# Performance work log

Measured on AMD Instinct MI355X. Metric: run time of the kernel, lower is better.

## Reference

```python
import jax, jax.numpy as jnp
import numpy as np

NT, NS, NH, NG, NR, NC = 365, 300, 128, 32, 8, 1


def _linear_params(key, fin, fout):
    k1, k2 = jax.random.split(key)
    s = 1.0 / np.sqrt(fin)
    W = jax.random.uniform(k1, (fout, fin), minval=-s, maxval=s, dtype=jnp.float32)
    b = jax.random.uniform(k2, (fout,), minval=-s, maxval=s, dtype=jnp.float32)
    return W, b


def setup_inputs() -> dict:
    key = jax.random.key(0)
    ks = jax.random.split(key, 9)
    x = jax.random.normal(ks[0], (NT, NS, 6), dtype=jnp.float32)
    xc = jax.random.normal(ks[1], (NS, NG), dtype=jnp.float32)
    fcR_w1, fcR_b1 = _linear_params(ks[2], NG, 256)
    fcR_w2, fcR_b2 = _linear_params(ks[3], 256, NH * NR)
    fcW_w1, fcW_b1 = _linear_params(ks[4], NG, 256)
    fcW_w2, fcW_b2 = _linear_params(ks[5], 256, NH * 7)
    fcT_w1, fcT_b1 = _linear_params(ks[6], 6 + NG, 256)
    fcT_w2, fcT_b2 = _linear_params(ks[7], 256, NH * 3)
    fcCT_w, fcCT_b = _linear_params(ks[8], 2 + NG, NC * NH * 3)
    return dict(x=x, xc=xc,
                fcR_w1=fcR_w1, fcR_b1=fcR_b1, fcR_w2=fcR_w2, fcR_b2=fcR_b2,
                fcW_w1=fcW_w1, fcW_b1=fcW_b1, fcW_w2=fcW_w2, fcW_b2=fcW_b2,
                fcT_w1=fcT_w1, fcT_b1=fcT_b1, fcT_w2=fcT_w2, fcT_b2=fcT_b2,
                fcCT_w=fcCT_w, fcCT_b=fcCT_b)


def _mlp(x, w1, b1, w2, b2):
    # Linear -> Tanh -> Dropout(identity in eval) -> Linear
    h = jnp.tanh(x @ w1.T + b1)
    return h @ w2.T + b2


def _conv_ts(q, r):
    # q: [nt, ns, nh]; r: [ns, nh, nr] routing weights. Causal temporal conv:
    # out[t] = sum_i q[t-i] * r[..., i]  (zero padded on the left)
    nt = q.shape[0]
    nr = r.shape[-1]
    qp = jnp.concatenate([jnp.zeros((nr - 1,) + q.shape[1:], q.dtype), q], axis=0)
    out = qp[nr - 1: nr - 1 + nt] * r[None, :, :, 0]
    for i in range(1, nr):
        out = out + qp[nr - 1 - i: nr - 1 - i + nt] * r[None, :, :, i]
    return out


def reference(x, xc, fcR_w1, fcR_b1, fcR_w2, fcR_b2,
              fcW_w1, fcW_b1, fcW_w2, fcW_b2,
              fcT_w1, fcT_b1, fcT_w2, fcT_b2,
              fcCT_w, fcCT_b):
    nh, nr = NH, NR
    P, E, T1, T2 = x[..., 0], x[..., 1], x[..., 2], x[..., 3]
    nt, ns = P.shape
    xcT = jnp.broadcast_to(xc[None], (nt, ns, xc.shape[-1]))
    xT = jnp.concatenate([x, xcT], axis=-1)                      # [nt, ns, 6+ng]

    # static gates per (site, bucket): sepPar with ['sigmoid']*4,'exp','relu','skip'
    w = _mlp(xc, fcW_w1, fcW_b1, fcW_w2, fcW_b2)                 # [ns, nh*7]
    kp = jax.nn.sigmoid(w[:, 0 * nh:1 * nh])
    ks_ = jax.nn.sigmoid(w[:, 1 * nh:2 * nh])
    kg = jax.nn.sigmoid(w[:, 2 * nh:3 * nh])
    gp = jax.nn.sigmoid(w[:, 3 * nh:4 * nh])
    gL = jnp.exp(w[:, 4 * nh:5 * nh]) * 2.0
    qb = jax.nn.relu(w[:, 5 * nh:6 * nh])
    ga = jax.nn.softmax(w[:, 6 * nh:7 * nh], axis=1)             # [ns, nh]

    # time-varying gates: ['skip','relu','exp']; vi overridden by hardsigmoid(v*2)
    v = _mlp(xT, fcT_w1, fcT_b1, fcT_w2, fcT_b2)                 # [nt, ns, nh*3]
    vi = jnp.clip(v[:, :, :nh] * 2.0 / 6.0 + 0.5, 0.0, 1.0)     # F.hardsigmoid(v*2)
    ve = jax.nn.relu(v[:, :, nh:2 * nh]) * 2.0
    vm = jnp.exp(v[:, :, 2 * nh:3 * nh])

    wR = _mlp(xc, fcR_w1, fcR_b1, fcR_w2, fcR_b2)                # [ns, nh*nr]
    r = jax.nn.relu(wR[:, :nh * nr]).reshape(ns, nh, nr)

    # snow fraction vf = arccos((T1+T2)/(T2-T1))/3.1415, overridden at extremes
    denom = T2 - T1
    ratio = jnp.clip((T1 + T2) / jnp.where(denom == 0, 1.0, denom), -1.0, 1.0)
    vf = jnp.arccos(ratio) / 3.1415
    vf = jnp.where(T1 >= 0, 0.0, jnp.where(T2 <= 0, 1.0, vf))
    Ps = P * vf                                                  # snow  [nt, ns]
    Pl = (P * (1.0 - vf))[:, :, None] * vi                       # rain  [nt, ns, nh]
    Ev = E[:, :, None] * ve                                      # evap  [nt, ns, nh]

    def step(carry, inp):
        Sf, Ss, Sg = carry
        Ps_k, Pl_k, Ev_k, vm_k = inp
        qf = jnp.minimum(Sf + Ps_k, vm_k)
        Sf = jax.nn.relu(Sf + Ps_k - vm_k)
        H = jax.nn.relu(Ss + Pl_k + qf - Ev_k)
        qp_ = jax.nn.relu(kp * (H - gL))
        qs = ks_ * jnp.minimum(H, gL)
        Ss = H - qp_ - qs
        qso = qs * (1.0 - gp)
        qsg = qs * gp
        qg = kg * (Sg + qsg) + qb
        Sg = (1.0 - kg) * (Sg + qsg) - qb
        return (Sf, Ss, Sg), (qp_, qso, qg)

    z = jnp.zeros((ns, nh), dtype=x.dtype)
    _, (Q1T, Q2T, Q3T) = jax.lax.scan(step, (z, z, z),
                                      (Ps[:, :, None], Pl, Ev, vm))

    Q1R = _conv_ts(Q1T, r)
    Q2R = _conv_ts(Q2T, r)
    Q3R = _conv_ts(Q3T, r)
    outQ = jnp.sum((Q1R + Q2R + Q3R) * ga, axis=2)               # [nt, ns]

    xTc = jnp.concatenate([T1[:, :, None], T2[:, :, None], xcT], axis=-1)
    wC = xTc @ fcCT_w.T + fcCT_b                                 # [nt, ns, nh*3]
    cp = jnp.exp(wC[:, :, 0 * nh:1 * nh])
    cs = jnp.exp(wC[:, :, 1 * nh:2 * nh])
    cg = jnp.exp(wC[:, :, 2 * nh:3 * nh])
    C1R = _conv_ts(Q1T * cp / 10.0, r)
    C2R = _conv_ts(Q2T * cs, r)
    C3R = _conv_ts(Q3T * cg, r)
    outC = jnp.sum((C1R + C2R + C3R) * ga, axis=2) / outQ
    return outQ, outC
```

## Files before the change

### kernel.cpp

```cpp
#include <hip/hip_runtime.h>
#include <math.h>

#define NTT 365
#define NSS 300
#define NROWS (NTT*NSS)
#define TROWS 416
#define SEGB 176

using bf16x8 = __attribute__((ext_vector_type(8))) short;
using f32x4  = __attribute__((ext_vector_type(4))) float;

__device__ __forceinline__ float sigf(float v) { return 1.0f / (1.0f + __expf(-v)); }

__device__ __forceinline__ float tanhfast(float x) {
    float e = __expf(2.0f * x);
    return 1.0f - 2.0f * __builtin_amdgcn_rcpf(1.0f + e);
}

__device__ __forceinline__ unsigned short f2bf(float f) {
    unsigned u = __builtin_bit_cast(unsigned, f);
    u += 0x7FFFu + ((u >> 16) & 1u);
    return (unsigned short)(u >> 16);
}

__global__ __launch_bounds__(256) void k_prep(const float* __restrict__ w1,
                                              const float* __restrict__ w2,
                                              unsigned short* __restrict__ w1s,
                                              unsigned short* __restrict__ w2s)
{
    int G = blockIdx.x * 256 + threadIdx.x;
    if (G < 2048) {
        int lane = G & 63, ks = (G >> 6) & 1, tile = G >> 7;
        int o = tile * 16 + (lane & 15);
        int kb = ks * 32 + (lane >> 4) * 8;
        unsigned short tmp[8];
#pragma unroll
        for (int e = 0; e < 8; ++e) {
            int k = kb + e;
            tmp[e] = (k < 38) ? f2bf(w1[o * 38 + k]) : (unsigned short)0;
        }
        *(bf16x8*)(w1s + (size_t)G * 8) = *(bf16x8*)tmp;
    } else if (G < 2048 + 12288) {
        int G2 = G - 2048;
        int lane = G2 & 63, ks = (G2 >> 6) & 7, tile = G2 >> 9;
        int o = tile * 16 + (lane & 15);
        int kb = ks * 32 + (lane >> 4) * 8;
        unsigned short tmp[8];
#pragma unroll
        for (int e = 0; e < 8; ++e) tmp[e] = f2bf(w2[o * 256 + kb + e]);
        *(bf16x8*)(w2s + (size_t)G2 * 8) = *(bf16x8*)tmp;
    }
}

__global__ __launch_bounds__(256) void k_site(
    const float* __restrict__ xc,
    const float* __restrict__ wW1, const float* __restrict__ bW1,
    const float* __restrict__ wW2, const float* __restrict__ bW2,
    const float* __restrict__ wR1, const float* __restrict__ bR1,
    const float* __restrict__ wR2, const float* __restrict__ bR2,
    float* __restrict__ wsite, float* __restrict__ rsite)
{
    __shared__ float xcb[10][32];
    __shared__ float hW[10][256];
    __shared__ float hR[10][256];
    int tid = threadIdx.x;
    int s0 = blockIdx.x * 10;
    int os = blockIdx.y;
    for (int i = tid; i < 10 * 32; i += 256) xcb[i / 32][i % 32] = xc[s0 * 32 + i];
    __syncthreads();
    {
        int j = tid;
        float aW[10], aR[10];
#pragma unroll
        for (int r = 0; r < 10; ++r) { aW[r] = bW1[j]; aR[r] = bR1[j]; }
        for (int k = 0; k < 32; ++k) {
            float wv = wW1[j * 32 + k], rv = wR1[j * 32 + k];
#pragma unroll
            for (int r = 0; r < 10; ++r) { float xv = xcb[r][k]; aW[r] += xv * wv; aR[r] += xv * rv; }
        }
#pragma unroll
        for (int r = 0; r < 10; ++r) { hW[r][j] = tanhfast(aW[r]); hR[r][j] = tanhfast(aR[r]); }
    }
    __syncthreads();
    if (tid < 240) {
        int o_lin = os * 240 + tid;
        float acc[10];
        if (o_lin < 896) {
            int o = o_lin;
#pragma unroll
            for (int r = 0; r < 10; ++r) acc[r] = bW2[o];
            for (int k = 0; k < 256; ++k) {
                float wv = wW2[o * 256 + k];
#pragma unroll
                for (int r = 0; r < 10; ++r) acc[r] += hW[r][k] * wv;
            }
#pragma unroll
            for (int r = 0; r < 10; ++r) wsite[(s0 + r) * 896 + o] = acc[r];
        } else {
            int o = o_lin - 896;
#pragma unroll
            for (int r = 0; r < 10; ++r) acc[r] = bR2[o];
            for (int k = 0; k < 256; ++k) {
                float wv = wR2[o * 256 + k];
#pragma unroll
                for (int r = 0; r < 10; ++r) acc[r] += hR[r][k] * wv;
            }
#pragma unroll
            for (int r = 0; r < 10; ++r) rsite[(s0 + r) * 1024 + o] = acc[r];
        }
    }
}

__global__ __launch_bounds__(128) void k_softmax_ga(const float* __restrict__ wsite,
                                                    float* __restrict__ ga)
{
    int s = blockIdx.x, tid = threadIdx.x;
    __shared__ float red[2];
    float v = wsite[s * 896 + 6 * 128 + tid];
    float m = v;
#pragma unroll
    for (int off = 32; off >= 1; off >>= 1) m = fmaxf(m, __shfl_xor(m, off));
    if ((tid & 63) == 0) red[tid >> 6] = m;
    __syncthreads();
    m = fmaxf(red[0], red[1]);
    __syncthreads();
    float e = __expf(v - m);
    float ssum = e;
#pragma unroll
    for (int off = 32; off >= 1; off >>= 1) ssum += __shfl_xor(ssum, off);
    if ((tid & 63) == 0) red[tid >> 6] = ssum;
    __syncthreads();
    ssum = red[0] + red[1];
    ga[s * 128 + tid] = e / ssum;
}

__global__ __launch_bounds__(128) void k_ct(const float* __restrict__ xc,
                                            const float* __restrict__ ctw,
                                            const float* __restrict__ ctb,
                                            float* __restrict__ ctp8,
                                            float* __restrict__ ctpb)
{
    __shared__ float xcs[32];
    int s = blockIdx.x, h = threadIdx.x;
    if (h < 32) xcs[h] = xc[s * 32 + h];
    __syncthreads();
    const float L2E = 1.4426950408889634f;
    const float LG01 = -3.3219280948873623f;
    float out[8];
    float cgb = 0.0f;
#pragma unroll
    for (int g = 0; g < 3; ++g) {
        const float* wr = ctw + (g * 128 + h) * 34;
        float base = ctb[g * 128 + h];
        for (int k = 0; k < 32; ++k) base += wr[2 + k] * xcs[k];
        float w0 = wr[0] * L2E, w1 = wr[1] * L2E;
        float bb = base * L2E + ((g == 0) ? LG01 : 0.0f);
        if (g == 0) { out[0] = w0; out[1] = w1; out[2] = bb; }
        else if (g == 1) { out[3] = w0; out[4] = w1; out[5] = bb; }
        else { out[6] = w0; out[7] = w1; cgb = bb; }
    }
    float4* dst = (float4*)(ctp8 + ((size_t)s * 128 + h) * 8);
    dst[0] = make_float4(out[0], out[1], out[2], out[3]);
    dst[1] = make_float4(out[4], out[5], out[6], out[7]);
    ctpb[(size_t)s * 128 + h] = cgb;
}

__global__ __launch_bounds__(512) void k_fcT(
    const float* __restrict__ x, const float* __restrict__ xc,
    const unsigned short* __restrict__ w1s, const float* __restrict__ b1,
    const unsigned short* __restrict__ w2s, const float* __restrict__ b2,
    float4* __restrict__ PT, unsigned* __restrict__ NVu)
{
    __shared__ unsigned short A1[64][72];
    __shared__ unsigned short hb[64][264];
    __shared__ float2 pfE[64];
    int tid = threadIdx.x;
    int row0 = blockIdx.x * 64;

    for (int idx = tid; idx < 64 * 64; idx += 512) {
        int r = idx >> 6, c = idx & 63;
        int g = row0 + r;
        float val = 0.0f;
        if (g < NROWS) {
            if (c < 6) val = x[g * 6 + c];
            else if (c < 38) { int s = g % NSS; val = xc[s * 32 + (c - 6)]; }
        }
        A1[r][c] = f2bf(val);
    }
    if (tid < 64) {
        int r = tid, g = row0 + r;
        float P = 0, E = 0, T1 = 0, T2 = 0;
        if (g < NROWS) { P = x[g * 6]; E = x[g * 6 + 1]; T1 = x[g * 6 + 2]; T2 = x[g * 6 + 3]; }
        float den = T2 - T1;
        float dg = (den == 0.0f) ? 1.0f : den;
        float ratio = fminf(fmaxf((T1 + T2) / dg, -1.0f), 1.0f);
        float vf = acosf(ratio) * (1.0f / 3.1415f);
        vf = (T1 >= 0.0f) ? 0.0f : ((T2 <= 0.0f) ? 1.0f : vf);
        pfE[r] = make_float2(P * (1.0f - vf), 2.0f * E);
        if (g < NROWS) PT[g] = make_float4(P * vf, T1, T2, vf);
    }
    __syncthreads();

    int lane = tid & 63, wv = tid >> 6;
    int r16 = lane & 15;
    int kg = (lane >> 4) * 8;
    int rq = (lane >> 4) * 4;

    {
        int mt = wv & 3, nb = (wv >> 2) * 8;
        f32x4 acc[8];
#pragma unroll
        for (int i = 0; i < 8; ++i) acc[i] = (f32x4){0.f, 0.f, 0.f, 0.f};
#pragma unroll
        for (int ks = 0; ks < 2; ++ks) {
            bf16x8 a = *(const bf16x8*)&A1[mt * 16 + r16][ks * 32 + kg];
#pragma unroll
            for (int i = 0; i < 8; ++i) {
                bf16x8 b = *(const bf16x8*)(w1s + ((size_t)(((nb + i) * 2 + ks) * 64 + lane) << 3));
                acc[i] = __builtin_amdgcn_mfma_f32_16x16x32_bf16(a, b, acc[i], 0, 0, 0);
            }
        }
#pragma unroll
        for (int i = 0; i < 8; ++i) {
            int col = (nb + i) * 16 + r16;
            float bias = b1[col];
#pragma unroll
            for (int j = 0; j < 4; ++j) {
                int row = mt * 16 + rq + j;
                hb[row][col] = f2bf(tanhfast(acc[i][j] + bias));
            }
        }
    }
    __syncthreads();

    {
        int t0 = wv, t1 = wv + 8, t2 = wv + 16;
        f32x4 acc[4][3];
#pragma unroll
        for (int m = 0; m < 4; ++m)
#pragma unroll
            for (int c = 0; c < 3; ++c) acc[m][c] = (f32x4){0.f, 0.f, 0.f, 0.f};
#pragma unroll
        for (int ks = 0; ks < 8; ++ks) {
            bf16x8 b0 = *(const bf16x8*)(w2s + ((size_t)((t0 * 8 + ks) * 64 + lane) << 3));
            bf16x8 b1v = *(const bf16x8*)(w2s + ((size_t)((t1 * 8 + ks) * 64 + lane) << 3));
            bf16x8 b2v = *(const bf16x8*)(w2s + ((size_t)((t2 * 8 + ks) * 64 + lane) << 3));
#pragma unroll
            for (int m = 0; m < 4; ++m) {
                bf16x8 a = *(const bf16x8*)&hb[m * 16 + r16][ks * 32 + kg];
                acc[m][0] = __builtin_amdgcn_mfma_f32_16x16x32_bf16(a, b0, acc[m][0], 0, 0, 0);
                acc[m][1] = __builtin_amdgcn_mfma_f32_16x16x32_bf16(a, b1v, acc[m][1], 0, 0, 0);
                acc[m][2] = __builtin_amdgcn_mfma_f32_16x16x32_bf16(a, b2v, acc[m][2], 0, 0, 0);
            }
        }
        int hcol = wv * 16 + r16;
        float bias0 = b2[hcol], bias1 = b2[128 + hcol], bias2 = b2[256 + hcol];
#pragma unroll
        for (int m = 0; m < 4; ++m) {
            float2 pf[4];
#pragma unroll
            for (int j = 0; j < 4; ++j) pf[j] = pfE[m * 16 + rq + j];
#pragma unroll
            for (int j = 0; j < 4; ++j) {
                int r = m * 16 + rq + j;
                int g = row0 + r;
                if (g < NROWS) {
                    float vi = fminf(fmaxf((acc[m][0][j] + bias0) * (1.0f / 3.0f) + 0.5f, 0.0f), 1.0f);
                    float pl = pf[j].x * vi;
                    float ev = pf[j].y * fmaxf(acc[m][1][j] + bias1, 0.0f);
                    float vmv = __expf(acc[m][2][j] + bias2);
                    unsigned pk = (unsigned)f2bf(pl - ev) | ((unsigned)f2bf(vmv) << 16);
                    NVu[(size_t)g * 128 + hcol] = pk;
                }
            }
        }
    }
}

__global__ __launch_bounds__(64) __attribute__((amdgpu_waves_per_eu(1, 2)))
void k_carry(const float* __restrict__ wsite,
             const float4* __restrict__ PTg, const unsigned* __restrict__ NVu,
             float4* __restrict__ chk)
{
    __shared__ float psl[192];
    int lane = threadIdx.x;
    int b = blockIdx.x;
    int lo = b & 7, q = b >> 3;
    int s = (q >> 1) * 8 + lo;
    int half = q & 1;
    if (s >= NSS) return;
    int h = half * 64 + lane;

    for (int t = lane; t < 192; t += 64) psl[t] = PTg[(size_t)t * NSS + s].x;

    const float* wrow = wsite + s * 896;
    float kp = sigf(wrow[0 * 128 + h]);
    float ks = sigf(wrow[1 * 128 + h]);
    float kg = sigf(wrow[2 * 128 + h]);
    float gp = sigf(wrow[3 * 128 + h]);
    float gL = __expf(wrow[4 * 128 + h]) * 2.0f;
    float kpgl = kp * gL;
    float qb = fmaxf(wrow[5 * 128 + h], 0.0f);

    const unsigned* nvbase = NVu + (size_t)s * 128 + h;
    unsigned A[16];
#pragma unroll
    for (int i = 0; i < 16; ++i) A[i] = nvbase[(size_t)i * (NSS * 128)];

    float Sf = 0.f, Ss = 0.f, Sg = 0.f;
    for (int tb = 0; tb < SEGB; tb += 16) {
#pragma unroll
        for (int u = 0; u < 16; ++u) {
            int t = tb + u;
            unsigned cur = A[u];
            A[u] = nvbase[(size_t)(t + 16) * (NSS * 128)];
            float psv = psl[t];
            float net = __builtin_bit_cast(float, cur << 16);
            float vm  = __builtin_bit_cast(float, cur & 0xFFFF0000u);
            float t1v = Sf + psv;
            float qf = fminf(t1v, vm);
            Sf = fmaxf(t1v - vm, 0.0f);
            float H = fmaxf(Ss + qf + net, 0.0f);
            float qp = fmaxf(kp * H - kpgl, 0.0f);
            float qs = ks * fminf(H, gL);
            Ss = H - qp - qs;
            float qsg = qs * gp;
            float tg2 = Sg + qsg;
            float qg = kg * tg2 + qb;
            Sg = tg2 - qg;
        }
        asm volatile("" ::: "memory");
    }
    chk[(size_t)s * 128 + h] = make_float4(Sf, Ss, Sg, 0.0f);
}

template<int ISC>
__device__ __forceinline__ void scan_body(
    int lane, int s, int half, int t0, int redFirst, float4 st0,
    float kp, float ks, float kg, float gp, float gpc, float gL, float kpgl, float qb,
    float r0, float r1, float r2, float r3, float r4, float r5, float r6, float r7,
    float c0, float c1, float c2, float c3, float c4, float c5,
    float c6, float c7, float c8,
    const unsigned* __restrict__ nvbase, const float4* ptlds, float (*red)[68],
    float* __restrict__ outp)
{
    float Sf = st0.x, Ss = st0.y, Sg = st0.z;
    float a0 = 0, a1 = 0, a2 = 0, a3 = 0, a4 = 0, a5 = 0, a6 = 0, a7 = 0;
    unsigned A[16], B[16];
#pragma unroll
    for (int i = 0; i < 16; ++i) A[i] = nvbase[(size_t)(t0 + i) * (NSS * 128)];
#pragma unroll
    for (int i = 0; i < 16; ++i) B[i] = nvbase[(size_t)(t0 + 16 + i) * (NSS * 128)];
    float4 pt[4];
#pragma unroll
    for (int i = 0; i < 4; ++i) pt[i] = ptlds[t0 + i];

    auto STEP = [&](int t, unsigned cur) {
        int ps = t & 3;
        float psv = pt[ps].x, T1 = pt[ps].y, T2 = pt[ps].z;
        pt[ps] = ptlds[t + 4];
        float net = __builtin_bit_cast(float, cur << 16);
        float vm  = __builtin_bit_cast(float, cur & 0xFFFF0000u);
        float t1v = Sf + psv;
        float qf = fminf(t1v, vm);
        Sf = fmaxf(t1v - vm, 0.0f);
        float H = fmaxf(Ss + qf + net, 0.0f);
        float qp = fmaxf(kp * H - kpgl, 0.0f);
        float qs = ks * fminf(H, gL);
        Ss = H - qp - qs;
        float qso = qs * gpc;
        float qsg = qs * gp;
        float tg2 = Sg + qsg;
        float qg = kg * tg2 + qb;
        Sg = tg2 - qg;
        float val;
        if (ISC) {
            float cp = exp2f(c0 * T1 + c1 * T2 + c2);
            float cs = exp2f(c3 * T1 + c4 * T2 + c5);
            float cg = exp2f(c6 * T1 + c7 * T2 + c8);
            val = qp * cp + qso * cs + qg * cg;
        } else {
            val = qp + qso + qg;
        }
        a0 += val * r0; a1 += val * r1; a2 += val * r2; a3 += val * r3;
        a4 += val * r4; a5 += val * r5; a6 += val * r6; a7 += val * r7;
        red[t & 15][lane] = a0;
        a0 = a1; a1 = a2; a2 = a3; a3 = a4; a4 = a5; a5 = a6; a6 = a7; a7 = 0.0f;
    };

    auto RED = [&](int base) {
        int v = lane >> 2, sub = lane & 3;
        const float4* rp4 = (const float4*)&red[v][0];
        float4 x0 = rp4[sub * 4 + 0];
        float4 x1 = rp4[sub * 4 + 1];
        float4 x2 = rp4[sub * 4 + 2];
        float4 x3 = rp4[sub * 4 + 3];
        float sA = (x0.x + x0.y) + (x0.z + x0.w);
        float sB = (x1.x + x1.y) + (x1.z + x1.w);
        float sC = (x2.x + x2.y) + (x2.z + x2.w);
        float sD = (x3.x + x3.y) + (x3.z + x3.w);
        float sm = (sA + sB) + (sC + sD);
        sm += __shfl_xor(sm, 1);
        sm += __shfl_xor(sm, 2);
        int tt = base + v;
        if (sub == 0 && tt < NTT)
            outp[((size_t)tt * NSS + s) * 2 + half] = sm;
    };

    for (int tb = 0; tb < 192; tb += 32) {
#pragma unroll
        for (int u = 0; u < 16; ++u) {
            int t = t0 + tb + u;
            unsigned cur = A[u];
            A[u] = nvbase[(size_t)(t + 32) * (NSS * 128)];
            STEP(t, cur);
        }
        asm volatile("" ::: "memory");
        if (redFirst | (tb > 0)) RED(t0 + tb);
#pragma unroll
        for (int u = 0; u < 16; ++u) {
            int t = t0 + tb + 16 + u;
            unsigned cur = B[u];
            B[u] = nvbase[(size_t)(t + 32) * (NSS * 128)];
            STEP(t, cur);
        }
        asm volatile("" ::: "memory");
        RED(t0 + tb + 16);
    }
}

__global__ __launch_bounds__(64) __attribute__((amdgpu_waves_per_eu(2, 4)))
void k_scan(
    const float* __restrict__ wsite, const float* __restrict__ rsite,
    const float* __restrict__ gaw,
    const float* __restrict__ ctp8, const float* __restrict__ ctpb,
    const float4* __restrict__ PTg, const unsigned* __restrict__ NVu,
    const float4* __restrict__ chk,
    float* __restrict__ pQ, float* __restrict__ pC)
{
    __shared__ float4 ptlds[TROWS];
    __shared__ __align__(16) float red[16][68];
    int lane = threadIdx.x;
    int b = blockIdx.x;
    int lo = b & 7, q = b >> 3;
    int s = (q >> 3) * 8 + lo;
    int half = (q >> 2) & 1;
    int role = (q >> 1) & 1;
    int seg  = q & 1;
    if (s >= NSS) return;
    int h = half * 64 + lane;

    for (int t = lane; t < TROWS; t += 64) ptlds[t] = PTg[(size_t)t * NSS + s];

    const float* wrow = wsite + s * 896;
    float kp = sigf(wrow[0 * 128 + h]);
    float ks = sigf(wrow[1 * 128 + h]);
    float kg = sigf(wrow[2 * 128 + h]);
    float gp = sigf(wrow[3 * 128 + h]);
    float gpc = 1.0f - gp;
    float gL = __expf(wrow[4 * 128 + h]) * 2.0f;
    float kpgl = kp * gL;
    float qb = fmaxf(wrow[5 * 128 + h], 0.0f);
    float ga = gaw[s * 128 + h];
    float4 rrA = *(const float4*)(rsite + s * 1024 + h * 8);
    float4 rrB = *(const float4*)(rsite + s * 1024 + h * 8 + 4);
    float r0 = fmaxf(rrA.x, 0.0f) * ga;
    float r1 = fmaxf(rrA.y, 0.0f) * ga;
    float r2 = fmaxf(rrA.z, 0.0f) * ga;
    float r3 = fmaxf(rrA.w, 0.0f) * ga;
    float r4 = fmaxf(rrB.x, 0.0f) * ga;
    float r5 = fmaxf(rrB.y, 0.0f) * ga;
    float r6 = fmaxf(rrB.z, 0.0f) * ga;
    float r7 = fmaxf(rrB.w, 0.0f) * ga;

    const unsigned* nvbase = NVu + (size_t)s * 128 + h;
    int t0 = seg ? SEGB : 0;
    int redFirst = seg ? 0 : 1;
    float4 st0 = seg ? chk[(size_t)s * 128 + h] : make_float4(0.f, 0.f, 0.f, 0.f);

    if (role == 0) {
        scan_body<0>(lane, s, half, t0, redFirst, st0,
                     kp, ks, kg, gp, gpc, gL, kpgl, qb,
                     r0, r1, r2, r3, r4, r5, r6, r7,
                     0.f, 0.f, 0.f, 0.f, 0.f, 0.f, 0.f, 0.f, 0.f,
                     nvbase, ptlds, red, pQ);
    } else {
        const float4* cp4 = (const float4*)(ctp8 + ((size_t)s * 128 + h) * 8);
        float4 cA = cp4[0], cB = cp4[1];
        float cgb = ctpb[(size_t)s * 128 + h];
        scan_body<1>(lane, s, half, t0, redFirst, st0,
                     kp, ks, kg, gp, gpc, gL, kpgl, qb,
                     r0, r1, r2, r3, r4, r5, r6, r7,
                     cA.x, cA.y, cA.z, cA.w, cB.x, cB.y, cB.z, cB.w, cgb,
                     nvbase, ptlds, red, pC);
    }
}

__global__ __launch_bounds__(256) void k_final(const float* __restrict__ pQ,
                                               const float* __restrict__ pC,
                                               float* __restrict__ out)
{
    int i = blockIdx.x * 256 + threadIdx.x;
    if (i < NROWS) {
        float q = pQ[i * 2] + pQ[i * 2 + 1];
        float c = pC[i * 2] + pC[i * 2 + 1];
        out[i] = q;
        out[NROWS + i] = c / q;
    }
}

extern "C" void kernel_launch(void* const* d_in, const int* in_sizes, int n_in,
                              void* d_out, int out_size, void* d_ws, size_t ws_size,
                              hipStream_t stream)
{
    const float* x      = (const float*)d_in[0];
    const float* xc     = (const float*)d_in[1];
    const float* fcR_w1 = (const float*)d_in[2];
    const float* fcR_b1 = (const float*)d_in[3];
    const float* fcR_w2 = (const float*)d_in[4];
    const float* fcR_b2 = (const float*)d_in[5];
    const float* fcW_w1 = (const float*)d_in[6];
    const float* fcW_b1 = (const float*)d_in[7];
    const float* fcW_w2 = (const float*)d_in[8];
    const float* fcW_b2 = (const float*)d_in[9];
    const float* fcT_w1 = (const float*)d_in[10];
    const float* fcT_b1 = (const float*)d_in[11];
    const float* fcT_w2 = (const float*)d_in[12];
    const float* fcT_b2 = (const float*)d_in[13];
    const float* fcCT_w = (const float*)d_in[14];
    const float* fcCT_b = (const float*)d_in[15];
    float* out = (float*)d_out;

    float* ws = (float*)d_ws;
    size_t o_w    = 0;
    size_t o_r    = o_w   + 300 * 896;
    size_t o_ga   = o_r   + 300 * 1024;
    size_t o_PT   = o_ga  + 300 * 128;
    size_t o_NV   = o_PT  + (size_t)TROWS * NSS * 4;
    size_t o_pQ   = o_NV  + (size_t)TROWS * NSS * 128;
    size_t o_pC   = o_pQ  + (size_t)NROWS * 2;
    size_t o_chk  = o_pC  + (size_t)NROWS * 2;
    size_t o_w1bf = o_chk + (size_t)300 * 128 * 4;
    size_t o_w2bf = o_w1bf + 8192;
    size_t o_ctp  = o_w2bf + 49152;
    size_t o_ctpb = o_ctp  + (size_t)300 * 128 * 8;

    float* wsite = ws + o_w;
    float* rsite = ws + o_r;
    float* gaw   = ws + o_ga;
    float4* PT   = (float4*)(ws + o_PT);
    unsigned* NVu = (unsigned*)(ws + o_NV);
    float* pQ    = ws + o_pQ;
    float* pC    = ws + o_pC;
    float4* chk  = (float4*)(ws + o_chk);
    unsigned short* w1s = (unsigned short*)(ws + o_w1bf);
    unsigned short* w2s = (unsigned short*)(ws + o_w2bf);
    float* ctp8  = ws + o_ctp;
    float* ctpb  = ws + o_ctpb;

    k_prep<<<56, 256, 0, stream>>>(fcT_w1, fcT_w2, w1s, w2s);
    k_site<<<dim3(30, 8), 256, 0, stream>>>(xc, fcW_w1, fcW_b1, fcW_w2, fcW_b2,
                                            fcR_w1, fcR_b1, fcR_w2, fcR_b2, wsite, rsite);
    k_softmax_ga<<<300, 128, 0, stream>>>(wsite, gaw);
    k_ct<<<300, 128, 0, stream>>>(xc, fcCT_w, fcCT_b, ctp8, ctpb);
    int nblk2 = (NROWS + 63) / 64;
    k_fcT<<<nblk2, 512, 0, stream>>>(x, xc, w1s, fcT_b1, w2s, fcT_b2, PT, NVu);
    k_carry<<<608, 64, 0, stream>>>(wsite, PT, NVu, chk);
    k_scan<<<2432, 64, 0, stream>>>(wsite, rsite, gaw, ctp8, ctpb,
                                    PT, NVu, chk, pQ, pC);
    k_final<<<(NROWS + 255) / 256, 256, 0, stream>>>(pQ, pC, out);
}
```

Measured before the change: 170.2 us.

## Split time scan into eight segments with multi-checkpoint carry and site-major NV layout

The carry kernel now runs the state recurrence over most of the series and writes state checkpoints every 48 steps. The scan kernel splits time into 8 segments (plus a one-group warmup overlap) instead of 2, and fuses the Q and C roles into one block, which doubles the block count. The NV buffer is re-laid out site/half-major with time contiguous in 64-wide rows, so each wave's per-step loads are contiguous. The aim is more parallelism and shorter serial chains in the scan, at the cost of a longer serial carry pass, duplicated recurrence work in the fused blocks, and a scattered-write layout in k_fcT.

```diff
diff --git a/kernel.cpp b/kernel.cpp
--- a/kernel.cpp
+++ b/kernel.cpp
@@ -5,7 +5,7 @@
 #define NSS 300
 #define NROWS (NTT*NSS)
 #define TROWS 416
-#define SEGB 176
+#define NCHK 7
 
 using bf16x8 = __attribute__((ext_vector_type(8))) short;
 using f32x4  = __attribute__((ext_vector_type(4))) float;
@@ -169,7 +169,7 @@
     const float* __restrict__ x, const float* __restrict__ xc,
     const unsigned short* __restrict__ w1s, const float* __restrict__ b1,
     const unsigned short* __restrict__ w2s, const float* __restrict__ b2,
-    float4* __restrict__ PT, unsigned* __restrict__ NVu)
+    float4* __restrict__ PT, unsigned* __restrict__ NV2)
 {
     __shared__ unsigned short A1[64][72];
     __shared__ unsigned short hb[64][264];
@@ -270,19 +270,20 @@
                     float ev = pf[j].y * fmaxf(acc[m][1][j] + bias1, 0.0f);
                     float vmv = __expf(acc[m][2][j] + bias2);
                     unsigned pk = (unsigned)f2bf(pl - ev) | ((unsigned)f2bf(vmv) << 16);
-                    NVu[(size_t)g * 128 + hcol] = pk;
+                    int tg = g / NSS, sg = g - tg * NSS;
+                    NV2[((size_t)(sg * 2 + (hcol >> 6)) * TROWS + tg) * 64 + (hcol & 63)] = pk;
                 }
             }
         }
     }
 }
 
-__global__ __launch_bounds__(64) __attribute__((amdgpu_waves_per_eu(1, 2)))
-void k_carry(const float* __restrict__ wsite,
-             const float4* __restrict__ PTg, const unsigned* __restrict__ NVu,
-             float4* __restrict__ chk)
-{
-    __shared__ float psl[192];
+__global__ __launch_bounds__(64) void k_carry(
+    const float* __restrict__ wsite,
+    const float4* __restrict__ PTg, const unsigned* __restrict__ NV2,
+    float4* __restrict__ chk)
+{
+    __shared__ float psl[352];
     int lane = threadIdx.x;
     int b = blockIdx.x;
     int lo = b & 7, q = b >> 3;
@@ -291,7 +292,7 @@
     if (s >= NSS) return;
     int h = half * 64 + lane;
 
-    for (int t = lane; t < 192; t += 64) psl[t] = PTg[(size_t)t * NSS + s].x;
+    for (int t = lane; t < 352; t += 64) psl[t] = PTg[(size_t)t * NSS + s].x;
 
     const float* wrow = wsite + s * 896;
     float kp = sigf(wrow[0 * 128 + h]);
@@ -302,63 +303,19 @@
     float kpgl = kp * gL;
     float qb = fmaxf(wrow[5 * 128 + h], 0.0f);
 
-    const unsigned* nvbase = NVu + (size_t)s * 128 + h;
-    unsigned A[16];
-#pragma unroll
-    for (int i = 0; i < 16; ++i) A[i] = nvbase[(size_t)i * (NSS * 128)];
+    const unsigned* nvp = NV2 + (size_t)(s * 2 + half) * TROWS * 64 + lane;
+    unsigned E[8], O[8];
+#pragma unroll
+    for (int u = 0; u < 8; ++u) E[u] = nvp[u * 64];
+#pragma unroll
+    for (int u = 0; u < 8; ++u) O[u] = nvp[(8 + u) * 64];
+    const unsigned* pf = nvp + 16 * 64;
 
     float Sf = 0.f, Ss = 0.f, Sg = 0.f;
-    for (int tb = 0; tb < SEGB; tb += 16) {
-#pragma unroll
-        for (int u = 0; u < 16; ++u) {
-            int t = tb + u;
-            unsigned cur = A[u];
-            A[u] = nvbase[(size_t)(t + 16) * (NSS * 128)];
-            float psv = psl[t];
-            float net = __builtin_bit_cast(float, cur << 16);
-            float vm  = __builtin_bit_cast(float, cur & 0xFFFF0000u);
-            float t1v = Sf + psv;
-            float qf = fminf(t1v, vm);
-            Sf = fmaxf(t1v - vm, 0.0f);
-            float H = fmaxf(Ss + qf + net, 0.0f);
-            float qp = fmaxf(kp * H - kpgl, 0.0f);
-            float qs = ks * fminf(H, gL);
-            Ss = H - qp - qs;
-            float qsg = qs * gp;
-            float tg2 = Sg + qsg;
-            float qg = kg * tg2 + qb;
-            Sg = tg2 - qg;
-        }
-        asm volatile("" ::: "memory");
-    }
-    chk[(size_t)s * 128 + h] = make_float4(Sf, Ss, Sg, 0.0f);
-}
-
-template<int ISC>
-__device__ __forceinline__ void scan_body(
-    int lane, int s, int half, int t0, int redFirst, float4 st0,
-    float kp, float ks, float kg, float gp, float gpc, float gL, float kpgl, float qb,
-    float r0, float r1, float r2, float r3, float r4, float r5, float r6, float r7,
-    float c0, float c1, float c2, float c3, float c4, float c5,
-    float c6, float c7, float c8,
-    const unsigned* __restrict__ nvbase, const float4* ptlds, float (*red)[68],
-    float* __restrict__ outp)
-{
-    float Sf = st0.x, Ss = st0.y, Sg = st0.z;
-    float a0 = 0, a1 = 0, a2 = 0, a3 = 0, a4 = 0, a5 = 0, a6 = 0, a7 = 0;
-    unsigned A[16], B[16];
-#pragma unroll
-    for (int i = 0; i < 16; ++i) A[i] = nvbase[(size_t)(t0 + i) * (NSS * 128)];
-#pragma unroll
-    for (int i = 0; i < 16; ++i) B[i] = nvbase[(size_t)(t0 + 16 + i) * (NSS * 128)];
-    float4 pt[4];
-#pragma unroll
-    for (int i = 0; i < 4; ++i) pt[i] = ptlds[t0 + i];
-
-    auto STEP = [&](int t, unsigned cur) {
-        int ps = t & 3;
-        float psv = pt[ps].x, T1 = pt[ps].y, T2 = pt[ps].z;
-        pt[ps] = ptlds[t + 4];
+    int nxt = 39, ci = 0;
+
+    auto CSTEP = [&](int t, unsigned cur) {
+        float psv = psl[t];
         float net = __builtin_bit_cast(float, cur << 16);
         float vm  = __builtin_bit_cast(float, cur & 0xFFFF0000u);
         float t1v = Sf + psv;
@@ -368,89 +325,54 @@
         float qp = fmaxf(kp * H - kpgl, 0.0f);
         float qs = ks * fminf(H, gL);
         Ss = H - qp - qs;
-        float qso = qs * gpc;
         float qsg = qs * gp;
         float tg2 = Sg + qsg;
         float qg = kg * tg2 + qb;
         Sg = tg2 - qg;
-        float val;
-        if (ISC) {
-            float cp = exp2f(c0 * T1 + c1 * T2 + c2);
-            float cs = exp2f(c3 * T1 + c4 * T2 + c5);
-            float cg = exp2f(c6 * T1 + c7 * T2 + c8);
-            val = qp * cp + qso * cs + qg * cg;
-        } else {
-            val = qp + qso + qg;
-        }
-        a0 += val * r0; a1 += val * r1; a2 += val * r2; a3 += val * r3;
-        a4 += val * r4; a5 += val * r5; a6 += val * r6; a7 += val * r7;
-        red[t & 15][lane] = a0;
-        a0 = a1; a1 = a2; a2 = a3; a3 = a4; a4 = a5; a5 = a6; a6 = a7; a7 = 0.0f;
+        if (t == nxt) {
+            chk[(size_t)ci * 38400 + (size_t)s * 128 + h] = make_float4(Sf, Ss, Sg, 0.f);
+            nxt += 48; ++ci;
+        }
     };
-
-    auto RED = [&](int base) {
-        int v = lane >> 2, sub = lane & 3;
-        const float4* rp4 = (const float4*)&red[v][0];
-        float4 x0 = rp4[sub * 4 + 0];
-        float4 x1 = rp4[sub * 4 + 1];
-        float4 x2 = rp4[sub * 4 + 2];
-        float4 x3 = rp4[sub * 4 + 3];
-        float sA = (x0.x + x0.y) + (x0.z + x0.w);
-        float sB = (x1.x + x1.y) + (x1.z + x1.w);
-        float sC = (x2.x + x2.y) + (x2.z + x2.w);
-        float sD = (x3.x + x3.y) + (x3.z + x3.w);
-        float sm = (sA + sB) + (sC + sD);
-        sm += __shfl_xor(sm, 1);
-        sm += __shfl_xor(sm, 2);
-        int tt = base + v;
-        if (sub == 0 && tt < NTT)
-            outp[((size_t)tt * NSS + s) * 2 + half] = sm;
+    auto CG = [&](unsigned (&X)[8], int tb) {
+#pragma unroll
+        for (int u = 0; u < 8; ++u) {
+            unsigned cur = X[u];
+            X[u] = pf[u * 64];
+            CSTEP(tb + u, cur);
+        }
+        pf += 512;
+        asm volatile("" ::: "memory");
     };
-
-    for (int tb = 0; tb < 192; tb += 32) {
-#pragma unroll
-        for (int u = 0; u < 16; ++u) {
-            int t = t0 + tb + u;
-            unsigned cur = A[u];
-            A[u] = nvbase[(size_t)(t + 32) * (NSS * 128)];
-            STEP(t, cur);
-        }
-        asm volatile("" ::: "memory");
-        if (redFirst | (tb > 0)) RED(t0 + tb);
-#pragma unroll
-        for (int u = 0; u < 16; ++u) {
-            int t = t0 + tb + 16 + u;
-            unsigned cur = B[u];
-            B[u] = nvbase[(size_t)(t + 32) * (NSS * 128)];
-            STEP(t, cur);
-        }
-        asm volatile("" ::: "memory");
-        RED(t0 + tb + 16);
-    }
-}
-
-__global__ __launch_bounds__(64) __attribute__((amdgpu_waves_per_eu(2, 4)))
-void k_scan(
+    int tb = 0;
+    for (int p = 0; p < 20; ++p) {
+        CG(E, tb); tb += 8;
+        CG(O, tb); tb += 8;
+    }
+    CG(E, tb);
+}
+
+__global__ __launch_bounds__(64) void k_scan(
     const float* __restrict__ wsite, const float* __restrict__ rsite,
     const float* __restrict__ gaw,
     const float* __restrict__ ctp8, const float* __restrict__ ctpb,
-    const float4* __restrict__ PTg, const unsigned* __restrict__ NVu,
+    const float4* __restrict__ PTg, const unsigned* __restrict__ NV2,
     const float4* __restrict__ chk,
     float* __restrict__ pQ, float* __restrict__ pC)
 {
-    __shared__ float4 ptlds[TROWS];
+    __shared__ float4 ptl[64];
     __shared__ __align__(16) float red[16][68];
     int lane = threadIdx.x;
     int b = blockIdx.x;
     int lo = b & 7, q = b >> 3;
-    int s = (q >> 3) * 8 + lo;
-    int half = (q >> 2) & 1;
-    int role = (q >> 1) & 1;
-    int seg  = q & 1;
+    int s = (q >> 4) * 8 + lo;
+    int half = (q >> 3) & 1;
+    int seg = q & 7;
     if (s >= NSS) return;
     int h = half * 64 + lane;
-
-    for (int t = lane; t < TROWS; t += 64) ptlds[t] = PTg[(size_t)t * NSS + s];
+    int t0 = seg ? (48 * seg - 8) : 0;
+
+    ptl[lane] = PTg[(size_t)(t0 + lane) * NSS + s];
 
     const float* wrow = wsite + s * 896;
     float kp = sigf(wrow[0 * 128 + h]);
@@ -472,28 +394,106 @@
     float r5 = fmaxf(rrB.y, 0.0f) * ga;
     float r6 = fmaxf(rrB.z, 0.0f) * ga;
     float r7 = fmaxf(rrB.w, 0.0f) * ga;
-
-    const unsigned* nvbase = NVu + (size_t)s * 128 + h;
-    int t0 = seg ? SEGB : 0;
-    int redFirst = seg ? 0 : 1;
-    float4 st0 = seg ? chk[(size_t)s * 128 + h] : make_float4(0.f, 0.f, 0.f, 0.f);
-
-    if (role == 0) {
-        scan_body<0>(lane, s, half, t0, redFirst, st0,
-                     kp, ks, kg, gp, gpc, gL, kpgl, qb,
-                     r0, r1, r2, r3, r4, r5, r6, r7,
-                     0.f, 0.f, 0.f, 0.f, 0.f, 0.f, 0.f, 0.f, 0.f,
-                     nvbase, ptlds, red, pQ);
-    } else {
-        const float4* cp4 = (const float4*)(ctp8 + ((size_t)s * 128 + h) * 8);
-        float4 cA = cp4[0], cB = cp4[1];
-        float cgb = ctpb[(size_t)s * 128 + h];
-        scan_body<1>(lane, s, half, t0, redFirst, st0,
-                     kp, ks, kg, gp, gpc, gL, kpgl, qb,
-                     r0, r1, r2, r3, r4, r5, r6, r7,
-                     cA.x, cA.y, cA.z, cA.w, cB.x, cB.y, cB.z, cB.w, cgb,
-                     nvbase, ptlds, red, pC);
-    }
+    const float4* cp4 = (const float4*)(ctp8 + ((size_t)s * 128 + h) * 8);
+    float4 cA = cp4[0], cB = cp4[1];
+    float c0 = cA.x, c1 = cA.y, c2 = cA.z, c3 = cA.w;
+    float c4 = cB.x, c5 = cB.y, c6 = cB.z, c7 = cB.w;
+    float c8 = ctpb[(size_t)s * 128 + h];
+
+    float Sf = 0.f, Ss = 0.f, Sg = 0.f;
+    if (seg) {
+        float4 st = chk[(size_t)(seg - 1) * 38400 + (size_t)s * 128 + h];
+        Sf = st.x; Ss = st.y; Sg = st.z;
+    }
+
+    const unsigned* nvp = NV2 + ((size_t)(s * 2 + half) * TROWS + t0) * 64 + lane;
+    unsigned E[8], O[8];
+#pragma unroll
+    for (int u = 0; u < 8; ++u) E[u] = nvp[u * 64];
+#pragma unroll
+    for (int u = 0; u < 8; ++u) O[u] = nvp[(8 + u) * 64];
+    const unsigned* pf = nvp + 16 * 64;
+
+    float4 pt[4];
+#pragma unroll
+    for (int i = 0; i < 4; ++i) pt[i] = ptl[i];
+
+    float aQ0 = 0, aQ1 = 0, aQ2 = 0, aQ3 = 0, aQ4 = 0, aQ5 = 0, aQ6 = 0, aQ7 = 0;
+    float aC0 = 0, aC1 = 0, aC2 = 0, aC3 = 0, aC4 = 0, aC5 = 0, aC6 = 0, aC7 = 0;
+
+    auto STEP = [&](int j, unsigned cur) {
+        int ps = j & 3;
+        float psv = pt[ps].x, T1 = pt[ps].y, T2 = pt[ps].z;
+        pt[ps] = ptl[j + 4];
+        float net = __builtin_bit_cast(float, cur << 16);
+        float vm  = __builtin_bit_cast(float, cur & 0xFFFF0000u);
+        float t1v = Sf + psv;
+        float qf = fminf(t1v, vm);
+        Sf = fmaxf(t1v - vm, 0.0f);
+        float H = fmaxf(Ss + qf + net, 0.0f);
+        float qp = fmaxf(kp * H - kpgl, 0.0f);
+        float qs = ks * fminf(H, gL);
+        Ss = H - qp - qs;
+        float qso = qs * gpc;
+        float qsg = qs * gp;
+        float tg2 = Sg + qsg;
+        float qg = kg * tg2 + qb;
+        Sg = tg2 - qg;
+        float valQ = qp + qso + qg;
+        float cpv = exp2f(c0 * T1 + c1 * T2 + c2);
+        float csv = exp2f(c3 * T1 + c4 * T2 + c5);
+        float cgv = exp2f(c6 * T1 + c7 * T2 + c8);
+        float valC = qp * cpv + qso * csv + qg * cgv;
+        aQ0 += valQ * r0; aQ1 += valQ * r1; aQ2 += valQ * r2; aQ3 += valQ * r3;
+        aQ4 += valQ * r4; aQ5 += valQ * r5; aQ6 += valQ * r6; aQ7 += valQ * r7;
+        aC0 += valC * r0; aC1 += valC * r1; aC2 += valC * r2; aC3 += valC * r3;
+        aC4 += valC * r4; aC5 += valC * r5; aC6 += valC * r6; aC7 += valC * r7;
+        red[j & 7][lane] = aQ0;
+        red[8 + (j & 7)][lane] = aC0;
+        aQ0 = aQ1; aQ1 = aQ2; aQ2 = aQ3; aQ3 = aQ4; aQ4 = aQ5; aQ5 = aQ6; aQ6 = aQ7; aQ7 = 0.0f;
+        aC0 = aC1; aC1 = aC2; aC2 = aC3; aC3 = aC4; aC4 = aC5; aC5 = aC6; aC6 = aC7; aC7 = 0.0f;
+    };
+
+    auto RED = [&](int tb) {
+        int v = lane >> 2, sub = lane & 3;
+        const float4* rp4 = (const float4*)&red[v][0];
+        float4 x0 = rp4[sub * 4 + 0];
+        float4 x1 = rp4[sub * 4 + 1];
+        float4 x2 = rp4[sub * 4 + 2];
+        float4 x3 = rp4[sub * 4 + 3];
+        float sA = (x0.x + x0.y) + (x0.z + x0.w);
+        float sB = (x1.x + x1.y) + (x1.z + x1.w);
+        float sC = (x2.x + x2.y) + (x2.z + x2.w);
+        float sD = (x3.x + x3.y) + (x3.z + x3.w);
+        float sm = (sA + sB) + (sC + sD);
+        sm += __shfl_xor(sm, 1);
+        sm += __shfl_xor(sm, 2);
+        int tt = t0 + tb + (v & 7);
+        if (sub == 0 && tt < NTT) {
+            float* bp = (v < 8) ? pQ : pC;
+            bp[((size_t)tt * NSS + s) * 2 + half] = sm;
+        }
+    };
+
+    auto GROUP = [&](unsigned (&X)[8], int TB, bool doRed) {
+#pragma unroll
+        for (int u = 0; u < 8; ++u) {
+            unsigned cur = X[u];
+            X[u] = pf[u * 64];
+            STEP(TB + u, cur);
+        }
+        pf += 512;
+        asm volatile("" ::: "memory");
+        if (doRed) RED(TB);
+    };
+
+    GROUP(E, 0, seg == 0);
+    GROUP(O, 8, true);
+    GROUP(E, 16, true);
+    GROUP(O, 24, true);
+    GROUP(E, 32, true);
+    GROUP(O, 40, true);
+    if (seg) GROUP(E, 48, true);
 }
 
 __global__ __launch_bounds__(256) void k_final(const float* __restrict__ pQ,
@@ -537,10 +537,10 @@
     size_t o_ga   = o_r   + 300 * 1024;
     size_t o_PT   = o_ga  + 300 * 128;
     size_t o_NV   = o_PT  + (size_t)TROWS * NSS * 4;
-    size_t o_pQ   = o_NV  + (size_t)TROWS * NSS * 128;
+    size_t o_pQ   = o_NV  + (size_t)300 * 2 * TROWS * 64;
     size_t o_pC   = o_pQ  + (size_t)NROWS * 2;
     size_t o_chk  = o_pC  + (size_t)NROWS * 2;
-    size_t o_w1bf = o_chk + (size_t)300 * 128 * 4;
+    size_t o_w1bf = o_chk + (size_t)NCHK * 38400 * 4;
     size_t o_w2bf = o_w1bf + 8192;
     size_t o_ctp  = o_w2bf + 49152;
     size_t o_ctpb = o_ctp  + (size_t)300 * 128 * 8;
@@ -549,7 +549,7 @@
     float* rsite = ws + o_r;
     float* gaw   = ws + o_ga;
     float4* PT   = (float4*)(ws + o_PT);
-    unsigned* NVu = (unsigned*)(ws + o_NV);
+    unsigned* NV2 = (unsigned*)(ws + o_NV);
     float* pQ    = ws + o_pQ;
     float* pC    = ws + o_pC;
     float4* chk  = (float4*)(ws + o_chk);
@@ -564,9 +564,9 @@
     k_softmax_ga<<<300, 128, 0, stream>>>(wsite, gaw);
     k_ct<<<300, 128, 0, stream>>>(xc, fcCT_w, fcCT_b, ctp8, ctpb);
     int nblk2 = (NROWS + 63) / 64;
-    k_fcT<<<nblk2, 512, 0, stream>>>(x, xc, w1s, fcT_b1, w2s, fcT_b2, PT, NVu);
-    k_carry<<<608, 64, 0, stream>>>(wsite, PT, NVu, chk);
-    k_scan<<<2432, 64, 0, stream>>>(wsite, rsite, gaw, ctp8, ctpb,
-                                    PT, NVu, chk, pQ, pC);
+    k_fcT<<<nblk2, 512, 0, stream>>>(x, xc, w1s, fcT_b1, w2s, fcT_b2, PT, NV2);
+    k_carry<<<608, 64, 0, stream>>>(wsite, PT, NV2, chk);
+    k_scan<<<4864, 64, 0, stream>>>(wsite, rsite, gaw, ctp8, ctpb,
+                                    PT, NV2, chk, pQ, pC);
     k_final<<<(NROWS + 255) / 256, 256, 0, stream>>>(pQ, pC, out);
 }
```

Result: no change. 169.1 us (-0.7%).
